# Kernel tuning notes

Measured on AMD Instinct MI355X. Metric: run time of the kernel, lower is better.

The kernel has to match this reference:

```python
import jax, jax.numpy as jnp
import numpy as np

B, S, E, D = 2, 1024, 1024, 2048
H, KV, HD = 8, 4, 256
SOFTCAP = 50.0
SCALE = 256.0 ** -0.5  # query_pre_attn_scalar ** -0.5
WINDOW = 512
EPS = 1e-6
THETA = 10000.0


def setup_inputs() -> dict:
    key = jax.random.key(0)
    ks = jax.random.split(key, 10)
    hidden_states = jax.random.normal(ks[0], (B, S, D), jnp.float32)
    encoder_hidden_states = jax.random.normal(ks[1], (B, E, D), jnp.float32)
    # two packed segments per sequence (position resets at S//2)
    position_ids = jnp.broadcast_to(
        jnp.concatenate([jnp.arange(S // 2), jnp.arange(S - S // 2)]), (B, S)
    ).astype(jnp.int32)
    decoder_attention_mask = jnp.ones((B, S), jnp.int32)
    encoder_attention_mask = jnp.broadcast_to(
        (jnp.arange(E) < (E - 64)).astype(jnp.int32), (B, E))
    # RoPE tables from position ids
    inv_freq = 1.0 / (THETA ** (jnp.arange(0, HD, 2, dtype=jnp.float32) / HD))
    freqs = position_ids.astype(jnp.float32)[..., None] * inv_freq  # [B,S,HD/2]
    emb = jnp.concatenate([freqs, freqs], axis=-1)  # [B,S,HD]
    cos, sin = jnp.cos(emb), jnp.sin(emb)
    wq = 0.02 * jax.random.normal(ks[2], (D, H * HD), jnp.float32)
    wk = 0.02 * jax.random.normal(ks[3], (D, KV * HD), jnp.float32)
    wv = 0.02 * jax.random.normal(ks[4], (D, KV * HD), jnp.float32)
    wo = 0.02 * jax.random.normal(ks[5], (H * HD, D), jnp.float32)
    q_norm_w = 0.1 * jax.random.normal(ks[6], (HD,), jnp.float32)
    k_norm_w = 0.1 * jax.random.normal(ks[7], (HD,), jnp.float32)
    return dict(hidden_states=hidden_states,
                encoder_hidden_states=encoder_hidden_states,
                cos=cos, sin=sin, wq=wq, wk=wk, wv=wv, wo=wo,
                q_norm_w=q_norm_w, k_norm_w=k_norm_w,
                decoder_attention_mask=decoder_attention_mask,
                encoder_attention_mask=encoder_attention_mask,
                position_ids=position_ids)


def _rms_norm(x, w):
    # GemmaRMSNorm: x * rsqrt(mean(x^2)+eps) * (1 + w)
    var = jnp.mean(x * x, axis=-1, keepdims=True)
    return x * jax.lax.rsqrt(var + EPS) * (1.0 + w)


def _rotate_half(x):
    h = x.shape[-1] // 2
    return jnp.concatenate([-x[..., h:], x[..., :h]], axis=-1)


def _build_merged_mask(dec_mask, enc_mask, position_ids):
    dm = dec_mask.astype(bool)
    em = enc_mask.astype(bool)
    Sq = dm.shape[1]
    causal = jnp.tril(jnp.ones((Sq, Sq), bool))
    # segment ids from non-increasing position resets (packing)
    reset = jnp.concatenate(
        [jnp.ones((dm.shape[0], 1), bool),
         position_ids[:, 1:] <= position_ids[:, :-1]], axis=1)
    seg = jnp.cumsum(reset.astype(jnp.int32), axis=1)
    block = seg[:, :, None] == seg[:, None, :]
    full_self = dm[:, None, :] & causal[None] & block  # [B,S,S]
    rows = jnp.arange(Sq)
    dist = rows[:, None] - rows[None, :]
    sliding = (dist >= 0) & (dist < WINDOW)
    self_mask = full_self & sliding[None]
    cross = jnp.broadcast_to(em[:, None, :], (dm.shape[0], Sq, em.shape[1]))
    return jnp.concatenate([self_mask, cross], axis=-1)[:, None]  # [B,1,S,S+E]


def reference(hidden_states, encoder_hidden_states, cos, sin, wq, wk, wv, wo,
              q_norm_w, k_norm_w, decoder_attention_mask,
              encoder_attention_mask, position_ids):
    Bq, Sq, _ = hidden_states.shape
    Ek = encoder_hidden_states.shape[1]
    q = (hidden_states @ wq).reshape(Bq, Sq, H, HD).transpose(0, 2, 1, 3)
    k_self = (hidden_states @ wk).reshape(Bq, Sq, KV, HD).transpose(0, 2, 1, 3)
    v_self = (hidden_states @ wv).reshape(Bq, Sq, KV, HD).transpose(0, 2, 1, 3)
    k_cross = (encoder_hidden_states @ wk).reshape(Bq, Ek, KV, HD).transpose(0, 2, 1, 3)
    v_cross = (encoder_hidden_states @ wv).reshape(Bq, Ek, KV, HD).transpose(0, 2, 1, 3)
    # QK RMSNorm (cross keys normalized but NOT rotated, matching source)
    q = _rms_norm(q, q_norm_w)
    k_self = _rms_norm(k_self, k_norm_w)
    k_cross = _rms_norm(k_cross, k_norm_w)
    c, s = cos[:, None, :, :], sin[:, None, :, :]
    q = q * c + _rotate_half(q) * s
    k_self = k_self * c + _rotate_half(k_self) * s
    k = jnp.concatenate([k_self, k_cross], axis=2)  # [B,KV,S+E,HD]
    v = jnp.concatenate([v_self, v_cross], axis=2)
    rep = H // KV
    k = jnp.repeat(k, rep, axis=1)
    v = jnp.repeat(v, rep, axis=1)
    mask = _build_merged_mask(decoder_attention_mask, encoder_attention_mask,
                              position_ids)
    scores = jnp.einsum('bhqd,bhkd->bhqk', q, k) * SCALE
    scores = SOFTCAP * jnp.tanh(scores / SOFTCAP)  # logit softcapping
    scores = jnp.where(mask, scores, jnp.float32(-1e30))
    attn = jax.nn.softmax(scores, axis=-1)
    out = jnp.einsum('bhqk,bhkd->bhqd', attn, v)
    out = out.transpose(0, 2, 1, 3).reshape(Bq, Sq, H * HD)
    return out @ wo
```

## Files before the change

kernel.cpp:

```cpp
#include <hip/hip_runtime.h>
#include <math.h>

#define B_ 2
#define S_ 1024
#define E_ 1024
#define D_ 2048
#define H_ 8
#define KV_ 4
#define HD_ 256
#define WINDOW_ 512u
#define SCALE_ 0.0625f
#define CAP_ 50.0f
#define EPS_ 1e-6f
#define CROSS_OK (-7)
#define KINV (-2147483647 - 1)

typedef __bf16 bf8_t __attribute__((ext_vector_type(8)));
typedef float fx4 __attribute__((ext_vector_type(4)));
#define MFMA16(a, b, c) __builtin_amdgcn_mfma_f32_16x16x32_bf16((a), (b), (c), 0, 0, 0)

typedef __attribute__((address_space(1))) unsigned int gas_u32;
typedef __attribute__((address_space(3))) unsigned int las_u32;
__device__ __forceinline__ void gl2lds16(const void* g, void* l) {
    __builtin_amdgcn_global_load_lds((const gas_u32*)g, (las_u32*)l, 16, 0, 0);
}

union U4 { __bf16 b[4]; unsigned long long u; };

__device__ __forceinline__ float pexp(float dot) {
    float e = __expf(dot * (2.0f * SCALE_ / CAP_));
    return __expf(-(2.0f * CAP_) / (e + 1.0f));
}

__device__ __forceinline__ void dev_tobf16(const float* __restrict__ x,
                                           __bf16* __restrict__ y, int n4, int i) {
    if (i >= n4) return;
    float4 v = ((const float4*)x)[i];
    U4 p;
    p.b[0] = (__bf16)v.x; p.b[1] = (__bf16)v.y;
    p.b[2] = (__bf16)v.z; p.b[3] = (__bf16)v.w;
    *(unsigned long long*)&y[(size_t)i * 4] = p.u;
}

__device__ __forceinline__ void dev_tsplit(const float* __restrict__ W,
                                           __bf16* __restrict__ Th,
                                           __bf16* __restrict__ Tl, int K, int N,
                                           int bx, int by, int t,
                                           float (*tile)[33], int wlo) {
    const int tx = t & 31, ty = t >> 5;
    const int k0 = bx * 32, n0 = by * 32;
#pragma unroll
    for (int r = 0; r < 4; ++r)
        tile[ty + r * 8][tx] = W[(size_t)(k0 + ty + r * 8) * N + n0 + tx];
    __syncthreads();
#pragma unroll
    for (int r = 0; r < 4; ++r) {
        float v = tile[tx][ty + r * 8];
        __bf16 h = (__bf16)v;
        size_t o = (size_t)(n0 + ty + r * 8) * K + k0 + tx;
        Th[o] = h;
        if (wlo) Tl[o] = (__bf16)(v - (float)h);
    }
}

__device__ __forceinline__ void dev_segscan(const int* __restrict__ pos,
                                            const int* __restrict__ dm,
                                            const int* __restrict__ em,
                                            int* __restrict__ seg,
                                            int* __restrict__ ki,
                                            int b, int t, int* wsum) {
    const int base = b * 1024 + t * 4;
    int4 p = *(const int4*)&pos[base];
    int pm1 = (t == 0) ? 0 : pos[base - 1];
    int r0 = (t == 0) ? 1 : (p.x <= pm1 ? 1 : 0);
    int r1 = (p.y <= p.x), r2 = (p.z <= p.y), r3 = (p.w <= p.z);
    int c0 = r0, c1 = c0 + r1, c2 = c1 + r2, c3 = c2 + r3;
    const int lane = t & 63, wv = t >> 6;
    int x = c3;
#pragma unroll
    for (int off = 1; off < 64; off <<= 1) {
        int y = __shfl_up(x, off, 64);
        if (lane >= off) x += y;
    }
    if (lane == 63) wsum[wv] = x;
    __syncthreads();
    int woff = 0;
#pragma unroll
    for (int w = 0; w < 4; ++w) if (w < wv) woff += wsum[w];
    const int excl = woff + x - c3;
    int sv[4] = {excl + c0, excl + c1, excl + c2, excl + c3};
    int4 dmv = *(const int4*)&dm[base];
    int4 emv = *(const int4*)&em[base];
    int dma[4] = {dmv.x, dmv.y, dmv.z, dmv.w};
    int ema[4] = {emv.x, emv.y, emv.z, emv.w};
#pragma unroll
    for (int r = 0; r < 4; ++r) {
        seg[base + r] = sv[r];
        ki[b * 2048 + t * 4 + r] = dma[r] ? sv[r] : KINV;
        ki[b * 2048 + 1024 + t * 4 + r] = ema[r] ? CROSS_OK : KINV;
    }
}

__global__ __launch_bounds__(256) void prep(
    const float* __restrict__ hs, const float* __restrict__ enc,
    const float* __restrict__ wq, const float* __restrict__ wk,
    const float* __restrict__ wvp, const float* __restrict__ wo,
    const int* __restrict__ pos, const int* __restrict__ dm,
    const int* __restrict__ em,
    __bf16* __restrict__ hs_bf, __bf16* __restrict__ enc_bf,
    __bf16* __restrict__ wqkvTH, __bf16* __restrict__ wqkvTL,
    __bf16* __restrict__ woTH, __bf16* __restrict__ woTL,
    int* __restrict__ seg, int* __restrict__ ki) {
    __shared__ float tile[32][33];
    __shared__ int wsum[4];
    int bid = blockIdx.x;
    const int t = threadIdx.x;
    if (bid < 4096) { dev_tobf16(hs, hs_bf, 1048576, bid * 256 + t); return; }
    bid -= 4096;
    if (bid < 4096) { dev_tobf16(enc, enc_bf, 1048576, bid * 256 + t); return; }
    bid -= 4096;
    if (bid < 4096) {
        dev_tsplit(wq, wqkvTH, nullptr, 2048, 2048, bid & 63, bid >> 6, t, tile, 0);
        return;
    }
    bid -= 4096;
    if (bid < 2048) {
        dev_tsplit(wk, wqkvTH + (size_t)2048 * 2048, nullptr, 2048, 1024,
                   bid & 63, bid >> 6, t, tile, 0);
        return;
    }
    bid -= 2048;
    if (bid < 2048) {
        dev_tsplit(wvp, wqkvTH + (size_t)3072 * 2048, wqkvTL + (size_t)3072 * 2048,
                   2048, 1024, bid & 63, bid >> 6, t, tile, 1);
        return;
    }
    bid -= 2048;
    if (bid < 4096) {
        dev_tsplit(wo, woTH, woTL, 2048, 2048, bid & 63, bid >> 6, t, tile, 1);
        return;
    }
    bid -= 4096;
    dev_segscan(pos, dm, em, seg, ki, bid, t, wsum);
}

template <int NPASS>
__device__ __forceinline__ void gemm_core2(
    const __bf16* __restrict__ Ah, const __bf16* __restrict__ Al,
    const __bf16* __restrict__ Bh, const __bf16* __restrict__ Bl,
    int row0, int col0, int K,
    __bf16* As0, __bf16* As1, __bf16* Bs0, __bf16* Bs1, fx4 (&acc)[4][4]) {
    const int tid = threadIdx.x, lane = tid & 63, wv = tid >> 6;
    const int l15 = lane & 15, lq = lane >> 4;
    const int wm = (wv >> 1) * 64, wn = (wv & 1) * 64;
    constexpr int WCNT = (NPASS == 1) ? 0x0F74 : (NPASS == 2) ? 0x0F76 : 0x0F78;

    auto stage = [&](int buf, int k0) {
#pragma unroll
        for (int s = 0; s < 2; ++s) {
            int ch = (wv * 2 + s) * 64 + lane;
            int r = ch >> 2, cp = ch & 3;
            int cl = (cp - ((r >> 1) & 3)) & 3;
            size_t ga = (size_t)(row0 + r) * K + k0 + cl * 8;
            size_t gb = (size_t)(col0 + r) * K + k0 + cl * 8;
            gl2lds16(Ah + ga, As0 + buf * 4096 + ch * 8);
            if (NPASS >= 3) gl2lds16(Al + ga, As1 + buf * 4096 + ch * 8);
            gl2lds16(Bh + gb, Bs0 + buf * 4096 + ch * 8);
            if (NPASS >= 2) gl2lds16(Bl + gb, Bs1 + buf * 4096 + ch * 8);
        }
    };

    stage(0, 0);
    for (int k0 = 0; k0 < K; k0 += 32) {
        const int buf = (k0 >> 5) & 1;
        const bool hasnext = (k0 + 32 < K);
        if (hasnext) stage(buf ^ 1, k0 + 32);
        if (hasnext) __builtin_amdgcn_s_waitcnt(WCNT);
        else         __builtin_amdgcn_s_waitcnt(0x0F70);
        __builtin_amdgcn_s_barrier();
        __builtin_amdgcn_sched_barrier(0);

        const __bf16* A0 = As0 + buf * 4096;
        const __bf16* A1 = As1 + buf * 4096;
        const __bf16* B0 = Bs0 + buf * 4096;
        const __bf16* B1 = Bs1 + buf * 4096;
        bf8_t ah[4], al[4], bh[4], bl[4];
#pragma unroll
        for (int i = 0; i < 4; ++i) {
            int row = wm + i * 16 + l15;
            int sl = row * 4 + ((lq + (row >> 1)) & 3);
            ah[i] = *(const bf8_t*)(A0 + sl * 8);
            if (NPASS >= 3) al[i] = *(const bf8_t*)(A1 + sl * 8);
        }
#pragma unroll
        for (int j = 0; j < 4; ++j) {
            int row = wn + j * 16 + l15;
            int sl = row * 4 + ((lq + (row >> 1)) & 3);
            bh[j] = *(const bf8_t*)(B0 + sl * 8);
            if (NPASS >= 2) bl[j] = *(const bf8_t*)(B1 + sl * 8);
        }
#pragma unroll
        for (int i = 0; i < 4; ++i)
#pragma unroll
            for (int j = 0; j < 4; ++j) {
                acc[i][j] = MFMA16(ah[i], bh[j], acc[i][j]);
                if (NPASS >= 2) acc[i][j] = MFMA16(ah[i], bl[j], acc[i][j]);
                if (NPASS >= 3) acc[i][j] = MFMA16(al[i], bh[j], acc[i][j]);
            }
        __builtin_amdgcn_sched_barrier(0);
        __builtin_amdgcn_s_barrier();
    }
}

__device__ __forceinline__ void gemm_core_half(
    const __bf16* __restrict__ Ah, const __bf16* __restrict__ Al,
    const __bf16* __restrict__ Bh, const __bf16* __restrict__ Bl,
    int row0, int col0, int K,
    __bf16* As0, __bf16* As1, __bf16* Bs0, __bf16* Bs1, fx4 (&acc)[4][2]) {
    const int tid = threadIdx.x, lane = tid & 63, wv = tid >> 6;
    const int l15 = lane & 15, lq = lane >> 4;
    const int wm = (wv >> 1) * 64, wn = (wv & 1) * 32;

    auto stage = [&](int buf, int k0) {
#pragma unroll
        for (int s = 0; s < 2; ++s) {
            int ch = s * 256 + tid;
            int r = ch >> 2, cp = ch & 3;
            int cl = (cp - ((r >> 1) & 3)) & 3;
            size_t ga = (size_t)(row0 + r) * K + k0 + cl * 8;
            gl2lds16(Ah + ga, As0 + buf * 4096 + ch * 8);
            gl2lds16(Al + ga, As1 + buf * 4096 + ch * 8);
        }
        {
            int ch = tid;
            int r = ch >> 2, cp = ch & 3;
            int cl = (cp - ((r >> 1) & 3)) & 3;
            size_t gb = (size_t)(col0 + r) * K + k0 + cl * 8;
            gl2lds16(Bh + gb, Bs0 + buf * 2048 + ch * 8);
            gl2lds16(Bl + gb, Bs1 + buf * 2048 + ch * 8);
        }
    };

    stage(0, 0);
    for (int k0 = 0; k0 < K; k0 += 32) {
        const int buf = (k0 >> 5) & 1;
        const bool hasnext = (k0 + 32 < K);
        if (hasnext) stage(buf ^ 1, k0 + 32);
        if (hasnext) __builtin_amdgcn_s_waitcnt(0x0F76);
        else         __builtin_amdgcn_s_waitcnt(0x0F70);
        __builtin_amdgcn_s_barrier();
        __builtin_amdgcn_sched_barrier(0);

        const __bf16* A0 = As0 + buf * 4096;
        const __bf16* A1 = As1 + buf * 4096;
        const __bf16* B0 = Bs0 + buf * 2048;
        const __bf16* B1 = Bs1 + buf * 2048;
        bf8_t ah[4], al[4], bh[2], bl[2];
#pragma unroll
        for (int i = 0; i < 4; ++i) {
            int row = wm + i * 16 + l15;
            int sl = row * 4 + ((lq + (row >> 1)) & 3);
            ah[i] = *(const bf8_t*)(A0 + sl * 8);
            al[i] = *(const bf8_t*)(A1 + sl * 8);
        }
#pragma unroll
        for (int j = 0; j < 2; ++j) {
            int row = wn + j * 16 + l15;
            int sl = row * 4 + ((lq + (row >> 1)) & 3);
            bh[j] = *(const bf8_t*)(B0 + sl * 8);
            bl[j] = *(const bf8_t*)(B1 + sl * 8);
        }
#pragma unroll
        for (int i = 0; i < 4; ++i)
#pragma unroll
            for (int j = 0; j < 2; ++j) {
                acc[i][j] = MFMA16(ah[i], bh[j], acc[i][j]);
                acc[i][j] = MFMA16(ah[i], bl[j], acc[i][j]);
                acc[i][j] = MFMA16(al[i], bh[j], acc[i][j]);
            }
        __builtin_amdgcn_sched_barrier(0);
        __builtin_amdgcn_s_barrier();
    }
}

__global__ __launch_bounds__(256) void gemm_proj(
    const __bf16* __restrict__ hsb, const __bf16* __restrict__ encb,
    const __bf16* __restrict__ BTh, const __bf16* __restrict__ BTl,
    float* __restrict__ qf32, float* __restrict__ ksf, float* __restrict__ kcf,
    __bf16* __restrict__ vtS, __bf16* __restrict__ vtC) {
    __shared__ __bf16 As0[8192], Bs0[8192], Bs1[8192];
    const int bx = blockIdx.x, row0 = blockIdx.y * 128;
    const __bf16* A;
    float* Ck; __bf16* Cv; int col0;
    if (bx < 32) { A = hsb;  col0 = bx * 128;               Ck = ksf; Cv = vtS; }
    else         { A = encb; col0 = (bx - 32) * 128 + 2048; Ck = kcf; Cv = vtC; }
    fx4 acc[4][4];
#pragma unroll
    for (int i = 0; i < 4; ++i)
#pragma unroll
        for (int j = 0; j < 4; ++j) acc[i][j] = (fx4){0.f, 0.f, 0.f, 0.f};
    if (col0 >= 3072)
        gemm_core2<2>(A, nullptr, BTh, BTl, row0, col0, D_, As0, nullptr, Bs0, Bs1, acc);
    else
        gemm_core2<1>(A, nullptr, BTh, BTl, row0, col0, D_, As0, nullptr, Bs0, Bs1, acc);

    const int tid = threadIdx.x, lane = tid & 63, wv = tid >> 6;
    const int l15 = lane & 15, lq = lane >> 4;
    const int wm = (wv >> 1) * 64, wn = (wv & 1) * 64;
    const int mode = (col0 < 2048) ? 0 : (col0 < 3072 ? 1 : 2);
#pragma unroll
    for (int i = 0; i < 4; ++i)
#pragma unroll
        for (int j = 0; j < 4; ++j) {
            int mb = row0 + wm + i * 16 + lq * 4;
            int n = col0 + wn + j * 16 + l15;
            if (mode == 0) {
#pragma unroll
                for (int r = 0; r < 4; ++r)
                    qf32[(size_t)(mb + r) * 2048 + n] = acc[i][j][r];
            } else if (mode == 1) {
                int nk = n - 2048;
#pragma unroll
                for (int r = 0; r < 4; ++r)
                    Ck[(size_t)(mb + r) * 1024 + nk] = acc[i][j][r];
            } else {
                int nv = n - 3072;
                int b = mb >> 10, s = mb & 1023;
                int kv = nv >> 8, d = nv & 255;
                U4 pk;
#pragma unroll
                for (int r = 0; r < 4; ++r) pk.b[r] = (__bf16)acc[i][j][r];
                *(unsigned long long*)&Cv[((size_t)(b * KV_ + kv) * HD_ + d) * 1024 + s] = pk.u;
            }
        }
}

__global__ __launch_bounds__(256) void gemm_out(
    const __bf16* __restrict__ Ah, const __bf16* __restrict__ Al,
    const __bf16* __restrict__ Bh, const __bf16* __restrict__ Bl,
    float* __restrict__ C) {
    __shared__ __bf16 As0[8192], As1[8192], Bs0[4096], Bs1[4096];
    const int row0 = blockIdx.y * 128, col0 = blockIdx.x * 64;
    fx4 acc[4][2];
#pragma unroll
    for (int i = 0; i < 4; ++i)
#pragma unroll
        for (int j = 0; j < 2; ++j) acc[i][j] = (fx4){0.f, 0.f, 0.f, 0.f};
    gemm_core_half(Ah, Al, Bh, Bl, row0, col0, 2048, As0, As1, Bs0, Bs1, acc);
    const int tid = threadIdx.x, lane = tid & 63, wv = tid >> 6;
    const int l15 = lane & 15, lq = lane >> 4;
    const int wm = (wv >> 1) * 64, wn = (wv & 1) * 32;
#pragma unroll
    for (int i = 0; i < 4; ++i)
#pragma unroll
        for (int j = 0; j < 2; ++j) {
            int mb = row0 + wm + i * 16 + lq * 4;
            int n = col0 + wn + j * 16 + l15;
#pragma unroll
            for (int r = 0; r < 4; ++r)
                C[(size_t)(mb + r) * 2048 + n] = acc[i][j][r];
        }
}

__global__ __launch_bounds__(256) void rms_all(
    const float* __restrict__ qf32, const float* __restrict__ ksf,
    const float* __restrict__ kcf,
    __bf16* __restrict__ q_bf, __bf16* __restrict__ k_bf,
    __bf16* __restrict__ kc_bf,
    const float* __restrict__ qnw, const float* __restrict__ knw,
    const float* __restrict__ cs, const float* __restrict__ sn) {
    int bid = blockIdx.x;
    const float* x; __bf16* out; const float* w;
    int nheads, do_rope, trans;
    if (bid < 16384)      { x = qf32; out = q_bf;  w = qnw; nheads = 8; do_rope = 1; trans = 0; }
    else if (bid < 24576) { bid -= 16384; x = ksf; out = k_bf;  w = knw; nheads = 4; do_rope = 1; trans = 1; }
    else                  { bid -= 24576; x = kcf; out = kc_bf; w = knw; nheads = 4; do_rope = 0; trans = 1; }
    const int tid = threadIdx.x;
    const size_t base = (size_t)bid * HD_;
    float v = x[base + tid];
    float ss = v * v;
#pragma unroll
    for (int off = 32; off; off >>= 1) ss += __shfl_down(ss, off);
    __shared__ float red[4];
    __shared__ float ybuf[HD_];
    const int lane = tid & 63, wvi = tid >> 6;
    if (lane == 0) red[wvi] = ss;
    __syncthreads();
    float tot = red[0] + red[1] + red[2] + red[3];
    float scale = rsqrtf(tot * (1.0f / HD_) + EPS_);
    float y = v * scale * (1.0f + w[tid]);
    const int m = bid / nheads;
    if (do_rope) {
        ybuf[tid] = y;
        __syncthreads();
        float rot = (tid < HD_ / 2) ? -ybuf[tid + HD_ / 2] : ybuf[tid - HD_ / 2];
        size_t coff = (size_t)m * HD_;
        y = y * cs[coff + tid] + rot * sn[coff + tid];
    }
    size_t oidx;
    if (trans) {
        int hh = bid % nheads;
        int b = m >> 10, s = m & 1023;
        oidx = ((size_t)(b * nheads + hh) * 1024 + s) * HD_ + tid;
    } else {
        oidx = base + tid;
    }
    out[oidx] = (__bf16)y;
}

__global__ __launch_bounds__(256, 1) void attn_part(
    const __bf16* __restrict__ qb,
    const __bf16* __restrict__ kb,
    const __bf16* __restrict__ kcb,
    const __bf16* __restrict__ vtS,
    const __bf16* __restrict__ vtC,
    const int* __restrict__ seg, const int* __restrict__ ki,
    float* __restrict__ accS, float* __restrict__ accC,
    float* __restrict__ lsS, float* __restrict__ lsC) {
    __shared__ __bf16 Ks[2][8192];
    __shared__ __bf16 Vs[2][8192];
    __shared__ __bf16 Ps[4][640];
    __shared__ int kinfoS[1600];
    const int tid = threadIdx.x, lane = tid & 63, wv = tid >> 6;
    const int l15 = lane & 15, lq = lane >> 4;
    const int bid = blockIdx.x;
    const int role = bid >> 8;
    const int g = bid & 7;
    const int b = g >> 2, kv = g & 3;
    const int idx = (bid >> 3) & 31;
    const int qt_raw = idx >> 1, h = kv * 2 + (idx & 1);
    const int qt = role ? (15 - qt_raw) : qt_raw;
    const int s0 = qt * 64;

    const int lo = (s0 >= 512) ? ((s0 - 511) & ~31) : 0;
    const int nts = (s0 + 64 - lo) >> 5;
    const int ccr = (33 - nts) >> 1;

    const __bf16* KbS = kb  + (size_t)(b * KV_ + kv) * (1024 * 256);
    const __bf16* VbS = vtS + (size_t)(b * KV_ + kv) * (256 * 1024);
    const __bf16* KbC = kcb + (size_t)(b * KV_ + kv) * (1024 * 256);
    const __bf16* VbC = vtC + (size_t)(b * KV_ + kv) * (256 * 1024);

    if (role == 0) {
        const int nk0 = nts * 32, nk1 = ccr * 32;
        for (int i = tid; i < nk0; i += 256) kinfoS[i] = ki[b * 2048 + lo + i];
        for (int i = tid; i < nk1; i += 256)
            kinfoS[nk0 + i] = ki[b * 2048 + 1024 + i];
    } else {
        const int nk1 = (32 - ccr) * 32;
        for (int i = tid; i < nk1; i += 256)
            kinfoS[i] = ki[b * 2048 + 1024 + ccr * 32 + i];
    }
    __syncthreads();

    const int qpos = s0 + wv * 16 + l15;
    bf8_t qf[8];
    const __bf16* qrow = qb + ((size_t)(b * S_ + qpos) * H_ + h) * HD_;
#pragma unroll
    for (int f = 0; f < 8; ++f) qf[f] = *(const bf8_t*)(qrow + f * 32 + lq * 8);
    const int segq = seg[b * S_ + qpos];

    fx4 accO[16];
#pragma unroll
    for (int j = 0; j < 16; ++j) accO[j] = (fx4){0.f, 0.f, 0.f, 0.f};
    float lsum = 0.f;
    const int swzk = l15 & 7;
    const int swzv = lq ^ ((l15 >> 1) & 3);

    const __bf16* phK[2]; const __bf16* phV[2];
    int phKey0[2], phKio[2], phNt[2], phSelf[2], nph;
    if (role == 0) {
        phK[0] = KbS; phV[0] = VbS; phKey0[0] = lo; phKio[0] = 0;
        phNt[0] = nts; phSelf[0] = 1;
        phK[1] = KbC; phV[1] = VbC; phKey0[1] = 0; phKio[1] = nts * 32;
        phNt[1] = ccr; phSelf[1] = 0;
        nph = 2;
    } else {
        phK[0] = KbC; phV[0] = VbC; phKey0[0] = ccr * 32; phKio[0] = 0;
        phNt[0] = 32 - ccr; phSelf[0] = 0;
        nph = 1;
    }

    for (int p = 0; p < nph; ++p) {
        const __bf16* Kb = phK[p];
        const __bf16* Vb = phV[p];
        const int key0 = phKey0[p], kiob = phKio[p], nt = phNt[p];
        const int selfm = phSelf[p];
        const int tgt = selfm ? segq : CROSS_OK;

        auto stage = [&](int buf, int t) {
            const __bf16* Kt = Kb + (size_t)(key0 + t * 32) * 256;
            const __bf16* Vt = Vb + (key0 + t * 32);
#pragma unroll
            for (int r = 0; r < 4; ++r) {
                int cid = r * 256 + tid;
                int key = cid >> 5, c = cid & 31;
                gl2lds16(Kt + key * 256 + (((c ^ (key & 7))) << 3), &Ks[buf][cid * 8]);
            }
#pragma unroll
            for (int r = 0; r < 4; ++r) {
                int cid = r * 256 + tid;
                int d = cid >> 2, kc = cid & 3;
                gl2lds16(Vt + (size_t)d * 1024 + ((kc ^ ((d >> 1) & 3)) << 3),
                         &Vs[buf][cid * 8]);
            }
        };

        stage(0, 0);
        for (int i = 0; i < nt; ++i) {
            const int kt0_c = key0 + i * 32;
            const int kio_c = kiob + i * 32;
            const bool hasnext = (i + 1 < nt);
            if (hasnext) stage((i + 1) & 1, i + 1);
            if (hasnext) __builtin_amdgcn_s_waitcnt(0x0F78);
            else         __builtin_amdgcn_s_waitcnt(0x0F70);
            __builtin_amdgcn_s_barrier();
            __builtin_amdgcn_sched_barrier(0);

            const __bf16* Ksb = Ks[i & 1];
            const __bf16* Vsb = Vs[i & 1];
            fx4 sc0 = (fx4){0.f, 0.f, 0.f, 0.f}, sc1 = (fx4){0.f, 0.f, 0.f, 0.f};
#pragma unroll
            for (int f = 0; f < 8; ++f) {
                bf8_t k0 = *(const bf8_t*)&Ksb[(l15 * 32 + ((f * 4 + lq) ^ swzk)) * 8];
                bf8_t k1 = *(const bf8_t*)&Ksb[((16 + l15) * 32 + ((f * 4 + lq) ^ swzk)) * 8];
                sc0 = MFMA16(k0, qf[f], sc0);
                sc1 = MFMA16(k1, qf[f], sc1);
            }
            int4 ki0 = *(const int4*)&kinfoS[kio_c + lq * 4];
            int4 ki1 = *(const int4*)&kinfoS[kio_c + 16 + lq * 4];
            int ka0[4] = {ki0.x, ki0.y, ki0.z, ki0.w};
            int ka1[4] = {ki1.x, ki1.y, ki1.z, ki1.w};
            U4 p0, p1;
#pragma unroll
            for (int r = 0; r < 4; ++r) {
                int key0r = kt0_c + lq * 4 + r;
                float e0 = pexp(sc0[r]);
                float e1 = pexp(sc1[r]);
                bool ok0 = (ka0[r] == tgt) &&
                           (!selfm || (unsigned)(qpos - key0r) < WINDOW_);
                bool ok1 = (ka1[r] == tgt) &&
                           (!selfm || (unsigned)(qpos - key0r - 16) < WINDOW_);
                float v0 = ok0 ? e0 : 0.f;
                float v1 = ok1 ? e1 : 0.f;
                lsum += v0 + v1;
                p0.b[r] = (__bf16)v0;
                p1.b[r] = (__bf16)v1;
            }
            *(unsigned long long*)&Ps[wv][l15 * 40 + lq * 4] = p0.u;
            *(unsigned long long*)&Ps[wv][l15 * 40 + 16 + lq * 4] = p1.u;
            bf8_t pf = *(const bf8_t*)&Ps[wv][l15 * 40 + lq * 8];
#pragma unroll
            for (int j = 0; j < 16; ++j) {
                bf8_t vb = *(const bf8_t*)&Vsb[((j * 16 + l15) * 4 + swzv) * 8];
                accO[j] = MFMA16(pf, vb, accO[j]);
            }
            __builtin_amdgcn_sched_barrier(0);
            __builtin_amdgcn_s_barrier();
        }
    }

    lsum += __shfl_xor(lsum, 16, 64);
    lsum += __shfl_xor(lsum, 32, 64);
    float* accT = role ? accC : accS;
    float* lsT  = role ? lsC  : lsS;
    if (lq == 0) lsT[(size_t)(b * S_ + qpos) * 8 + h] = lsum;
#pragma unroll
    for (int j = 0; j < 16; ++j)
#pragma unroll
        for (int r = 0; r < 4; ++r) {
            size_t idx2 = (size_t)(b * S_ + s0 + wv * 16 + lq * 4 + r) * 2048 +
                          h * 256 + j * 16 + l15;
            accT[idx2] = accO[j][r];
        }
}

__global__ __launch_bounds__(256) void combine(
    const float* __restrict__ aS, const float* __restrict__ aC,
    const float* __restrict__ lS, const float* __restrict__ lC,
    __bf16* __restrict__ aH, __bf16* __restrict__ aL) {
    int i = blockIdx.x * 256 + threadIdx.x;
    size_t base = (size_t)i * 4;
    int row = (int)(base >> 11);
    int h = (int)((base >> 8) & 7);
    float inv = 1.0f / (lS[row * 8 + h] + lC[row * 8 + h]);
    float4 a = ((const float4*)aS)[i];
    float4 c = ((const float4*)aC)[i];
    float o[4] = {(a.x + c.x) * inv, (a.y + c.y) * inv,
                  (a.z + c.z) * inv, (a.w + c.w) * inv};
    U4 ph, pl;
#pragma unroll
    for (int r = 0; r < 4; ++r) {
        __bf16 hi = (__bf16)o[r];
        ph.b[r] = hi;
        pl.b[r] = (__bf16)(o[r] - (float)hi);
    }
    *(unsigned long long*)&aH[base] = ph.u;
    *(unsigned long long*)&aL[base] = pl.u;
}

extern "C" void kernel_launch(void* const* d_in, const int* in_sizes, int n_in,
                              void* d_out, int out_size, void* d_ws, size_t ws_size,
                              hipStream_t stream) {
    (void)in_sizes; (void)n_in; (void)out_size; (void)ws_size;
    const float* hs  = (const float*)d_in[0];
    const float* enc = (const float*)d_in[1];
    const float* cs  = (const float*)d_in[2];
    const float* sn  = (const float*)d_in[3];
    const float* wq  = (const float*)d_in[4];
    const float* wk  = (const float*)d_in[5];
    const float* wv  = (const float*)d_in[6];
    const float* wo  = (const float*)d_in[7];
    const float* qnw = (const float*)d_in[8];
    const float* knw = (const float*)d_in[9];
    const int* dm    = (const int*)d_in[10];
    const int* em    = (const int*)d_in[11];
    const int* pos   = (const int*)d_in[12];
    float* out = (float*)d_out;

    char* ws = (char*)d_ws;
    const size_t MB = 1ull << 20;
    __bf16* hs_bf   = (__bf16*)(ws + 0 * MB);
    __bf16* enc_bf  = (__bf16*)(ws + 8 * MB);
    __bf16* wqkvTH  = (__bf16*)(ws + 16 * MB);
    __bf16* wqkvTL  = (__bf16*)(ws + 32 * MB);
    __bf16* woTH    = (__bf16*)(ws + 48 * MB);
    __bf16* woTL    = (__bf16*)(ws + 56 * MB);
    float*  qf32    = (float*)(ws + 64 * MB);
    float*  ksf     = (float*)(ws + 80 * MB);
    float*  kcf     = (float*)(ws + 88 * MB);
    __bf16* k_bf    = (__bf16*)(ws + 104 * MB);
    __bf16* kc_bf   = (__bf16*)(ws + 108 * MB);
    __bf16* vtS     = (__bf16*)(ws + 112 * MB);
    __bf16* vtC     = (__bf16*)(ws + 116 * MB);
    int*    seg     = (int*)(ws + 120 * MB);
    int*    kinfo   = (int*)(ws + 121 * MB);
    __bf16* q_bf    = (__bf16*)(ws + 124 * MB);
    __bf16* aoutH   = (__bf16*)(ws + 0 * MB);
    __bf16* aoutL   = (__bf16*)(ws + 9 * MB);
    float*  accS    = (float*)(ws + 64 * MB);
    float*  accC    = (float*)(ws + 81 * MB);
    float*  lsS     = (float*)(ws + 98 * MB);
    float*  lsC     = (float*)(ws + 99 * MB);

    prep<<<20482, 256, 0, stream>>>(hs, enc, wq, wk, wv, wo, pos, dm, em,
                                    hs_bf, enc_bf, wqkvTH, wqkvTL, woTH, woTL,
                                    seg, kinfo);

    gemm_proj<<<dim3(48, 16), 256, 0, stream>>>(hs_bf, enc_bf, wqkvTH, wqkvTL,
                                                qf32, ksf, kcf, vtS, vtC);

    rms_all<<<32768, 256, 0, stream>>>(qf32, ksf, kcf, q_bf, k_bf, kc_bf,
                                       qnw, knw, cs, sn);

    attn_part<<<512, 256, 0, stream>>>(q_bf, k_bf, kc_bf, vtS, vtC, seg, kinfo,
                                       accS, accC, lsS, lsC);
    combine<<<4096, 256, 0, stream>>>(accS, accC, lsS, lsC, aoutH, aoutL);

    gemm_out<<<dim3(32, 16), 256, 0, stream>>>(aoutH, aoutL, woTH, woTL, out);
}
```

Baseline: 388.5 us.

## Fuse split-attention combine into attn_part via atomic flags; vectorize RMSNorm per wave

The separate combine kernel is removed. Each self/cross attention block now stores its partial results and bumps a per-region atomic counter, and whichever block finishes second reads the other's partial accumulator and sum, normalizes, and writes the hi/lo bf16 output directly. The prep kernel gets an extra block that zeroes the flags. RMSNorm+RoPE is also rewritten so that one wave handles one row with float4 loads and shuffle-based reduction and rotation, which drops the shared-memory barriers and cuts the block count fourfold. The fusion saves a launch and one full pass over the fp32 partials, but it adds atomics, fences and a serialized tail on the last-finishing block.

```diff
diff --git a/kernel.cpp b/kernel.cpp
--- a/kernel.cpp
+++ b/kernel.cpp
@@ -110,7 +110,7 @@
     __bf16* __restrict__ hs_bf, __bf16* __restrict__ enc_bf,
     __bf16* __restrict__ wqkvTH, __bf16* __restrict__ wqkvTL,
     __bf16* __restrict__ woTH, __bf16* __restrict__ woTL,
-    int* __restrict__ seg, int* __restrict__ ki) {
+    int* __restrict__ seg, int* __restrict__ ki, int* __restrict__ flags) {
     __shared__ float tile[32][33];
     __shared__ int wsum[4];
     int bid = blockIdx.x;
@@ -141,7 +141,8 @@
         return;
     }
     bid -= 4096;
-    dev_segscan(pos, dm, em, seg, ki, bid, t, wsum);
+    if (bid < 2) { dev_segscan(pos, dm, em, seg, ki, bid, t, wsum); return; }
+    flags[t] = 0;
 }
 
 template <int NPASS>
@@ -369,43 +370,50 @@
     __bf16* __restrict__ kc_bf,
     const float* __restrict__ qnw, const float* __restrict__ knw,
     const float* __restrict__ cs, const float* __restrict__ sn) {
-    int bid = blockIdx.x;
+    const int t = threadIdx.x, wvi = t >> 6, lane = t & 63;
+    const int row = blockIdx.x * 4 + wvi;
     const float* x; __bf16* out; const float* w;
-    int nheads, do_rope, trans;
-    if (bid < 16384)      { x = qf32; out = q_bf;  w = qnw; nheads = 8; do_rope = 1; trans = 0; }
-    else if (bid < 24576) { bid -= 16384; x = ksf; out = k_bf;  w = knw; nheads = 4; do_rope = 1; trans = 1; }
-    else                  { bid -= 24576; x = kcf; out = kc_bf; w = knw; nheads = 4; do_rope = 0; trans = 1; }
-    const int tid = threadIdx.x;
-    const size_t base = (size_t)bid * HD_;
-    float v = x[base + tid];
-    float ss = v * v;
-#pragma unroll
-    for (int off = 32; off; off >>= 1) ss += __shfl_down(ss, off);
-    __shared__ float red[4];
-    __shared__ float ybuf[HD_];
-    const int lane = tid & 63, wvi = tid >> 6;
-    if (lane == 0) red[wvi] = ss;
-    __syncthreads();
-    float tot = red[0] + red[1] + red[2] + red[3];
-    float scale = rsqrtf(tot * (1.0f / HD_) + EPS_);
-    float y = v * scale * (1.0f + w[tid]);
-    const int m = bid / nheads;
+    int nsh, do_rope, trans, rbase;
+    if (row < 16384)      { rbase = row;         x = qf32; out = q_bf;  w = qnw; nsh = 3; do_rope = 1; trans = 0; }
+    else if (row < 24576) { rbase = row - 16384; x = ksf;  out = k_bf;  w = knw; nsh = 2; do_rope = 1; trans = 1; }
+    else                  { rbase = row - 24576; x = kcf;  out = kc_bf; w = knw; nsh = 2; do_rope = 0; trans = 1; }
+    float4 v = ((const float4*)x)[(size_t)rbase * 64 + lane];
+    float ss = v.x * v.x + v.y * v.y + v.z * v.z + v.w * v.w;
+#pragma unroll
+    for (int off = 32; off; off >>= 1) ss += __shfl_xor(ss, off, 64);
+    float scale = rsqrtf(ss * (1.0f / HD_) + EPS_);
+    float4 w4 = ((const float4*)w)[lane];
+    float y0 = v.x * scale * (1.0f + w4.x);
+    float y1 = v.y * scale * (1.0f + w4.y);
+    float y2 = v.z * scale * (1.0f + w4.z);
+    float y3 = v.w * scale * (1.0f + w4.w);
+    const int m = rbase >> nsh;
     if (do_rope) {
-        ybuf[tid] = y;
-        __syncthreads();
-        float rot = (tid < HD_ / 2) ? -ybuf[tid + HD_ / 2] : ybuf[tid - HD_ / 2];
-        size_t coff = (size_t)m * HD_;
-        y = y * cs[coff + tid] + rot * sn[coff + tid];
+        float r0 = __shfl_xor(y0, 32, 64);
+        float r1 = __shfl_xor(y1, 32, 64);
+        float r2 = __shfl_xor(y2, 32, 64);
+        float r3 = __shfl_xor(y3, 32, 64);
+        float sg = (lane < 32) ? -1.0f : 1.0f;
+        float4 c4 = ((const float4*)cs)[(size_t)m * 64 + lane];
+        float4 s4 = ((const float4*)sn)[(size_t)m * 64 + lane];
+        y0 = y0 * c4.x + sg * r0 * s4.x;
+        y1 = y1 * c4.y + sg * r1 * s4.y;
+        y2 = y2 * c4.z + sg * r2 * s4.z;
+        y3 = y3 * c4.w + sg * r3 * s4.w;
     }
     size_t oidx;
     if (trans) {
-        int hh = bid % nheads;
+        int nh = 1 << nsh;
+        int hh = rbase & (nh - 1);
         int b = m >> 10, s = m & 1023;
-        oidx = ((size_t)(b * nheads + hh) * 1024 + s) * HD_ + tid;
+        oidx = ((size_t)(b * nh + hh) * 1024 + s) * HD_ + lane * 4;
     } else {
-        oidx = base + tid;
-    }
-    out[oidx] = (__bf16)y;
+        oidx = (size_t)rbase * HD_ + lane * 4;
+    }
+    U4 pk;
+    pk.b[0] = (__bf16)y0; pk.b[1] = (__bf16)y1;
+    pk.b[2] = (__bf16)y2; pk.b[3] = (__bf16)y3;
+    *(unsigned long long*)&out[oidx] = pk.u;
 }
 
 __global__ __launch_bounds__(256, 1) void attn_part(
@@ -416,11 +424,14 @@
     const __bf16* __restrict__ vtC,
     const int* __restrict__ seg, const int* __restrict__ ki,
     float* __restrict__ accS, float* __restrict__ accC,
-    float* __restrict__ lsS, float* __restrict__ lsC) {
+    float* __restrict__ lsS, float* __restrict__ lsC,
+    int* __restrict__ flags,
+    __bf16* __restrict__ aH, __bf16* __restrict__ aL) {
     __shared__ __bf16 Ks[2][8192];
     __shared__ __bf16 Vs[2][8192];
     __shared__ __bf16 Ps[4][640];
     __shared__ int kinfoS[1600];
+    __shared__ int oldS;
     const int tid = threadIdx.x, lane = tid & 63, wv = tid >> 6;
     const int l15 = lane & 15, lq = lane >> 4;
     const int bid = blockIdx.x;
@@ -573,30 +584,35 @@
                           h * 256 + j * 16 + l15;
             accT[idx2] = accO[j][r];
         }
-}
-
-__global__ __launch_bounds__(256) void combine(
-    const float* __restrict__ aS, const float* __restrict__ aC,
-    const float* __restrict__ lS, const float* __restrict__ lC,
-    __bf16* __restrict__ aH, __bf16* __restrict__ aL) {
-    int i = blockIdx.x * 256 + threadIdx.x;
-    size_t base = (size_t)i * 4;
-    int row = (int)(base >> 11);
-    int h = (int)((base >> 8) & 7);
-    float inv = 1.0f / (lS[row * 8 + h] + lC[row * 8 + h]);
-    float4 a = ((const float4*)aS)[i];
-    float4 c = ((const float4*)aC)[i];
-    float o[4] = {(a.x + c.x) * inv, (a.y + c.y) * inv,
-                  (a.z + c.z) * inv, (a.w + c.w) * inv};
-    U4 ph, pl;
-#pragma unroll
-    for (int r = 0; r < 4; ++r) {
-        __bf16 hi = (__bf16)o[r];
-        ph.b[r] = hi;
-        pl.b[r] = (__bf16)(o[r] - (float)hi);
-    }
-    *(unsigned long long*)&aH[base] = ph.u;
-    *(unsigned long long*)&aL[base] = pl.u;
+
+    const int rgn = (((b * KV_ + kv) * 2 + (idx & 1)) << 4) + qt;
+    __syncthreads();
+    __threadfence();
+    if (tid == 0)
+        oldS = __hip_atomic_fetch_add(&flags[rgn], 1, __ATOMIC_ACQ_REL,
+                                      __HIP_MEMORY_SCOPE_AGENT);
+    __syncthreads();
+    if (oldS == 1) {
+        __threadfence();
+        const float* accP = role ? accS : accC;
+        const float* lsP  = role ? lsS  : lsC;
+        float lother = lsP[(size_t)(b * S_ + qpos) * 8 + h];
+        float tot = lsum + lother;
+        float inv[4];
+#pragma unroll
+        for (int r = 0; r < 4; ++r) inv[r] = 1.0f / __shfl(tot, lq * 4 + r, 64);
+#pragma unroll
+        for (int j = 0; j < 16; ++j)
+#pragma unroll
+            for (int r = 0; r < 4; ++r) {
+                size_t idx2 = (size_t)(b * S_ + s0 + wv * 16 + lq * 4 + r) * 2048 +
+                              h * 256 + j * 16 + l15;
+                float o = (accO[j][r] + accP[idx2]) * inv[r];
+                __bf16 hi = (__bf16)o;
+                aH[idx2] = hi;
+                aL[idx2] = (__bf16)(o - (float)hi);
+            }
+    }
 }
 
 extern "C" void kernel_launch(void* const* d_in, const int* in_sizes, int n_in,
@@ -642,20 +658,20 @@
     float*  accC    = (float*)(ws + 81 * MB);
     float*  lsS     = (float*)(ws + 98 * MB);
     float*  lsC     = (float*)(ws + 99 * MB);
-
-    prep<<<20482, 256, 0, stream>>>(hs, enc, wq, wk, wv, wo, pos, dm, em,
+    int*    flags   = (int*)(ws + 100 * MB);
+
+    prep<<<20483, 256, 0, stream>>>(hs, enc, wq, wk, wv, wo, pos, dm, em,
                                     hs_bf, enc_bf, wqkvTH, wqkvTL, woTH, woTL,
-                                    seg, kinfo);
+                                    seg, kinfo, flags);
 
     gemm_proj<<<dim3(48, 16), 256, 0, stream>>>(hs_bf, enc_bf, wqkvTH, wqkvTL,
                                                 qf32, ksf, kcf, vtS, vtC);
 
-    rms_all<<<32768, 256, 0, stream>>>(qf32, ksf, kcf, q_bf, k_bf, kc_bf,
-                                       qnw, knw, cs, sn);
+    rms_all<<<8192, 256, 0, stream>>>(qf32, ksf, kcf, q_bf, k_bf, kc_bf,
+                                      qnw, knw, cs, sn);
 
     attn_part<<<512, 256, 0, stream>>>(q_bf, k_bf, kc_bf, vtS, vtC, seg, kinfo,
-                                       accS, accC, lsS, lsC);
-    combine<<<4096, 256, 0, stream>>>(accS, accC, lsS, lsC, aoutH, aoutL);
+                                       accS, accC, lsS, lsC, flags, aoutH, aoutL);
 
     gemm_out<<<dim3(32, 16), 256, 0, stream>>>(aoutH, aoutL, woTH, woTL, out);
 }
```

After: 498.3 us. +28.3%, slower.
